# Optimization experiments

Measured on AMD Instinct MI355X. Metric: run time of the kernel, lower is better.

## Reference

```python
import jax, jax.numpy as jnp
import numpy as np

N_HEADS = 8


def setup_inputs() -> dict:
    key = jax.random.key(0)
    qkv = jax.random.normal(key, (4, 1536, 2048), dtype=jnp.float32)
    return {"qkv": qkv}


def reference(qkv):
    bs, width, length = qkv.shape
    assert width % (3 * N_HEADS) == 0
    ch = width // (3 * N_HEADS)
    q, k, v = jnp.split(qkv, 3, axis=1)            # each [bs, H*C, T]
    scale = 1.0 / (ch ** 0.25)                      # 1/sqrt(sqrt(ch)) applied to both q and k
    q = (q * scale).reshape(bs * N_HEADS, ch, length)
    k = (k * scale).reshape(bs * N_HEADS, ch, length)
    v = v.reshape(bs * N_HEADS, ch, length)
    weight = jnp.einsum('bct,bcs->bts', q, k)       # [bs*H, T, T]
    weight = jax.nn.softmax(weight.astype(jnp.float32), axis=-1).astype(weight.dtype)
    a = jnp.einsum('bts,bcs->bct', weight, v)       # [bs*H, C, T]
    return a.reshape(bs, -1, length)
```

## Files before the change

kernel.cpp:

```cpp
#include <hip/hip_runtime.h>


typedef _Float16 half8  __attribute__((ext_vector_type(8)));
typedef _Float16 half4  __attribute__((ext_vector_type(4)));
typedef float    floatx4 __attribute__((ext_vector_type(4)));

constexpr int T   = 2048;
constexpr int TQ  = 128;
constexpr int TS  = 64;
constexpr int LDK = 72;
constexpr int LDV = 72;
constexpr int LDP = 72;
constexpr int NIT = T / TS;
constexpr float QSCALE = 0.125f * 1.44269504088896340736f;

__device__ __forceinline__ float pick4(float t0, float t1, float t2, float t3, int rr) {
    return (rr & 2) ? ((rr & 1) ? t3 : t2) : ((rr & 1) ? t1 : t0);
}
__device__ __forceinline__ half4 pack4(float a, float b, float c, float d) {
    half4 r;
    r[0] = (_Float16)a; r[1] = (_Float16)b;
    r[2] = (_Float16)c; r[3] = (_Float16)d;
    return r;
}

__global__ __launch_bounds__(512, 4)
void qkv_attn_kernel(const float* __restrict__ qkv, float* __restrict__ out) {
    __shared__ __align__(16) _Float16 sK[2][TS * LDK];
    __shared__ __align__(16) _Float16 sV[2][64 * LDV];
    __shared__ __align__(16) _Float16 sP[TQ * LDP];

    const int tid  = threadIdx.x;
    const int wave = tid >> 6;
    const int lane = tid & 63;
    const int n16  = lane & 15;
    const int quad = lane >> 4;

    const int bx = blockIdx.x;
    const int h  = bx & 31;
    const int qt = bx >> 5;
    const int b  = h >> 3;
    const int hh = h & 7;
    const int q0 = qt * TQ;

    const float* __restrict__ qbase = qkv + (size_t)(b * 1536 + hh * 64) * T;
    const float* __restrict__ kbase = qkv + (size_t)(b * 1536 + 512 + hh * 64) * T;
    const float* __restrict__ vbase = qkv + (size_t)(b * 1536 + 1024 + hh * 64) * T;
    float* __restrict__ obase = out + (size_t)(b * 512 + hh * 64) * T;

    const bool producer = wave >= 4;

    const int ptid = tid & 255;
    const int ks   = ((ptid >> 6) << 4) | (ptid & 15);
    const int kc4  = ((ptid >> 4) & 3) << 2;
    const int vc   = ptid >> 4;
    const int vs4  = (ptid & 15) << 2;

    auto stage = [&](int buf, int s0) {
        _Float16* kd = &sK[buf][ks * LDK];
        const float* kg = kbase + s0 + ks;
#pragma unroll
        for (int i = 0; i < 4; ++i) {
            const int c = i * 16 + kc4;
            const float f0 = kg[(c + 0) * T];
            const float f1 = kg[(c + 1) * T];
            const float f2 = kg[(c + 2) * T];
            const float f3 = kg[(c + 3) * T];
            *(half4*)&kd[c] = pack4(f0, f1, f2, f3);
        }
        const float* vg = vbase + vc * T + s0 + vs4;
        _Float16* vd = &sV[buf][vc * LDV + vs4];
#pragma unroll
        for (int i = 0; i < 4; ++i) {
            const floatx4 vv = *(const floatx4*)&vg[i * 16 * T];
            *(half4*)&vd[i * 16 * LDV] = pack4(vv.x, vv.y, vv.z, vv.w);
        }
    };

    half8 aq[2][2];
    floatx4 oacc[4][2];
    float lsum[2][4];

    if (!producer) {
#pragma unroll
        for (int qtile = 0; qtile < 2; ++qtile) {
            const int q = q0 + wave * 32 + qtile * 16 + n16;
#pragma unroll
            for (int kc = 0; kc < 2; ++kc)
#pragma unroll
                for (int j = 0; j < 8; ++j) {
                    const int c = kc * 32 + quad * 8 + j;
                    aq[qtile][kc][j] = (_Float16)(qbase[c * T + q] * QSCALE);
                }
        }
#pragma unroll
        for (int mt = 0; mt < 4; ++mt)
#pragma unroll
            for (int qtile = 0; qtile < 2; ++qtile) oacc[mt][qtile] = (floatx4)(0.f);
#pragma unroll
        for (int qtile = 0; qtile < 2; ++qtile)
#pragma unroll
            for (int r = 0; r < 4; ++r) lsum[qtile][r] = 0.f;
    }

    if (producer) stage(0, 0);
    __syncthreads();

    for (int it = 0; it < NIT; ++it) {
        const int buf = it & 1;
        if (producer) {
            if (it + 1 < NIT) stage(buf ^ 1, (it + 1) * TS);
        } else {
            const _Float16* kb = &sK[buf][0];
            const _Float16* vb = &sV[buf][0];
#pragma unroll
            for (int qtile = 0; qtile < 2; ++qtile) {
                floatx4 sacc[4];
#pragma unroll
                for (int stile = 0; stile < 4; ++stile) {
                    const half8 bk0 = *(const half8*)&kb[(stile * 16 + n16) * LDK + quad * 8];
                    const half8 bk1 = *(const half8*)&kb[(stile * 16 + n16) * LDK + 32 + quad * 8];
                    floatx4 acc = (floatx4)(0.f);
                    acc = __builtin_amdgcn_mfma_f32_16x16x32_f16(aq[qtile][0], bk0, acc, 0, 0, 0);
                    acc = __builtin_amdgcn_mfma_f32_16x16x32_f16(aq[qtile][1], bk1, acc, 0, 0, 0);
                    sacc[stile] = acc;
                }
#pragma unroll
                for (int stile = 0; stile < 4; ++stile)
#pragma unroll
                    for (int r = 0; r < 4; ++r) {
                        const float pv = __builtin_amdgcn_exp2f(sacc[stile][r]);
                        lsum[qtile][r] += pv;
                        sP[(wave * 32 + qtile * 16 + quad * 4 + r) * LDP + stile * 16 + n16] =
                            (_Float16)pv;
                    }
            }
#pragma unroll
            for (int kc = 0; kc < 2; ++kc) {
                const half8 bp0 = *(const half8*)&sP[(wave * 32 + n16) * LDP + kc * 32 + quad * 8];
                const half8 bp1 = *(const half8*)&sP[(wave * 32 + 16 + n16) * LDP + kc * 32 + quad * 8];
#pragma unroll
                for (int mt = 0; mt < 4; ++mt) {
                    const half8 av = *(const half8*)&vb[(mt * 16 + n16) * LDV + kc * 32 + quad * 8];
                    oacc[mt][0] = __builtin_amdgcn_mfma_f32_16x16x32_f16(av, bp0, oacc[mt][0], 0, 0, 0);
                    oacc[mt][1] = __builtin_amdgcn_mfma_f32_16x16x32_f16(av, bp1, oacc[mt][1], 0, 0, 0);
                }
            }
        }
        __syncthreads();
    }

    if (!producer) {
#pragma unroll
        for (int qtile = 0; qtile < 2; ++qtile) {
            float l0 = lsum[qtile][0], l1 = lsum[qtile][1];
            float l2 = lsum[qtile][2], l3 = lsum[qtile][3];
#pragma unroll
            for (int msk = 1; msk < 16; msk <<= 1) {
                l0 += __shfl_xor(l0, msk);
                l1 += __shfl_xor(l1, msk);
                l2 += __shfl_xor(l2, msk);
                l3 += __shfl_xor(l3, msk);
            }
            const int srcl = (n16 >> 2) << 4;
            const float t0 = __shfl(l0, srcl);
            const float t1 = __shfl(l1, srcl);
            const float t2 = __shfl(l2, srcl);
            const float t3 = __shfl(l3, srcl);
            const float linv = 1.0f / pick4(t0, t1, t2, t3, n16 & 3);
            const int tcol = q0 + wave * 32 + qtile * 16 + n16;
#pragma unroll
            for (int mt = 0; mt < 4; ++mt)
#pragma unroll
                for (int r = 0; r < 4; ++r)
                    obase[(mt * 16 + quad * 4 + r) * T + tcol] = oacc[mt][qtile][r] * linv;
        }
    }
}

extern "C" void kernel_launch(void* const* d_in, const int* in_sizes, int n_in,
                              void* d_out, int out_size, void* d_ws, size_t ws_size,
                              hipStream_t stream) {
    const float* qkv = (const float*)d_in[0];
    float* out = (float*)d_out;
    qkv_attn_kernel<<<dim3(512), dim3(512), 0, stream>>>(qkv, out);
}
```

Before: 132.3 us.

## Keep softmax probabilities in registers by transposing the QK^T MFMA operand order

```diff
diff --git a/kernel.cpp b/kernel.cpp
--- a/kernel.cpp
+++ b/kernel.cpp
@@ -10,13 +10,9 @@
 constexpr int TS  = 64;
 constexpr int LDK = 72;
 constexpr int LDV = 72;
-constexpr int LDP = 72;
 constexpr int NIT = T / TS;
 constexpr float QSCALE = 0.125f * 1.44269504088896340736f;
 
-__device__ __forceinline__ float pick4(float t0, float t1, float t2, float t3, int rr) {
-    return (rr & 2) ? ((rr & 1) ? t3 : t2) : ((rr & 1) ? t1 : t0);
-}
 __device__ __forceinline__ half4 pack4(float a, float b, float c, float d) {
     half4 r;
     r[0] = (_Float16)a; r[1] = (_Float16)b;
@@ -28,13 +24,12 @@
 void qkv_attn_kernel(const float* __restrict__ qkv, float* __restrict__ out) {
     __shared__ __align__(16) _Float16 sK[2][TS * LDK];
     __shared__ __align__(16) _Float16 sV[2][64 * LDV];
-    __shared__ __align__(16) _Float16 sP[TQ * LDP];
 
     const int tid  = threadIdx.x;
     const int wave = tid >> 6;
     const int lane = tid & 63;
     const int n16  = lane & 15;
-    const int quad = lane >> 4;
+    const int g    = lane >> 4;
 
     const int bx = blockIdx.x;
     const int h  = bx & 31;
@@ -77,30 +72,27 @@
         }
     };
 
-    half8 aq[2][2];
+    half8 bq[2][2];
     floatx4 oacc[4][2];
-    float lsum[2][4];
+    float lsum[2];
 
     if (!producer) {
 #pragma unroll
-        for (int qtile = 0; qtile < 2; ++qtile) {
-            const int q = q0 + wave * 32 + qtile * 16 + n16;
+        for (int qt2 = 0; qt2 < 2; ++qt2) {
+            const int q = q0 + wave * 32 + qt2 * 16 + n16;
 #pragma unroll
-            for (int kc = 0; kc < 2; ++kc)
+            for (int kcA = 0; kcA < 2; ++kcA)
 #pragma unroll
                 for (int j = 0; j < 8; ++j) {
-                    const int c = kc * 32 + quad * 8 + j;
-                    aq[qtile][kc][j] = (_Float16)(qbase[c * T + q] * QSCALE);
+                    const int c = kcA * 32 + g * 8 + j;
+                    bq[qt2][kcA][j] = (_Float16)(qbase[c * T + q] * QSCALE);
                 }
         }
 #pragma unroll
         for (int mt = 0; mt < 4; ++mt)
 #pragma unroll
-            for (int qtile = 0; qtile < 2; ++qtile) oacc[mt][qtile] = (floatx4)(0.f);
-#pragma unroll
-        for (int qtile = 0; qtile < 2; ++qtile)
-#pragma unroll
-            for (int r = 0; r < 4; ++r) lsum[qtile][r] = 0.f;
+            for (int qt2 = 0; qt2 < 2; ++qt2) oacc[mt][qt2] = (floatx4)(0.f);
+        lsum[0] = 0.f; lsum[1] = 0.f;
     }
 
     if (producer) stage(0, 0);
@@ -114,36 +106,47 @@
             const _Float16* kb = &sK[buf][0];
             const _Float16* vb = &sV[buf][0];
 #pragma unroll
-            for (int qtile = 0; qtile < 2; ++qtile) {
-                floatx4 sacc[4];
+            for (int kc2 = 0; kc2 < 2; ++kc2) {
+                floatx4 sacc[2][2];
 #pragma unroll
-                for (int stile = 0; stile < 4; ++stile) {
-                    const half8 bk0 = *(const half8*)&kb[(stile * 16 + n16) * LDK + quad * 8];
-                    const half8 bk1 = *(const half8*)&kb[(stile * 16 + n16) * LDK + 32 + quad * 8];
-                    floatx4 acc = (floatx4)(0.f);
-                    acc = __builtin_amdgcn_mfma_f32_16x16x32_f16(aq[qtile][0], bk0, acc, 0, 0, 0);
-                    acc = __builtin_amdgcn_mfma_f32_16x16x32_f16(aq[qtile][1], bk1, acc, 0, 0, 0);
-                    sacc[stile] = acc;
+                for (int sub = 0; sub < 2; ++sub) {
+                    const int stile = kc2 * 2 + sub;
+                    const half8 ak0 = *(const half8*)&kb[(stile * 16 + n16) * LDK + g * 8];
+                    const half8 ak1 = *(const half8*)&kb[(stile * 16 + n16) * LDK + 32 + g * 8];
+#pragma unroll
+                    for (int qt2 = 0; qt2 < 2; ++qt2) {
+                        floatx4 acc = (floatx4)(0.f);
+                        acc = __builtin_amdgcn_mfma_f32_16x16x32_f16(ak0, bq[qt2][0], acc, 0, 0, 0);
+                        acc = __builtin_amdgcn_mfma_f32_16x16x32_f16(ak1, bq[qt2][1], acc, 0, 0, 0);
+                        sacc[qt2][sub] = acc;
+                    }
+                }
+                half8 av[4];
+#pragma unroll
+                for (int mt = 0; mt < 4; ++mt) {
+                    const _Float16* vr = &vb[(mt * 16 + n16) * LDV + kc2 * 32];
+                    const half4 lo = *(const half4*)&vr[g * 4];
+                    const half4 hi = *(const half4*)&vr[16 + g * 4];
+                    av[mt][0] = lo[0]; av[mt][1] = lo[1]; av[mt][2] = lo[2]; av[mt][3] = lo[3];
+                    av[mt][4] = hi[0]; av[mt][5] = hi[1]; av[mt][6] = hi[2]; av[mt][7] = hi[3];
                 }
 #pragma unroll
-                for (int stile = 0; stile < 4; ++stile)
+                for (int qt2 = 0; qt2 < 2; ++qt2) {
+                    float pv[8];
 #pragma unroll
-                    for (int r = 0; r < 4; ++r) {
-                        const float pv = __builtin_amdgcn_exp2f(sacc[stile][r]);
-                        lsum[qtile][r] += pv;
-                        sP[(wave * 32 + qtile * 16 + quad * 4 + r) * LDP + stile * 16 + n16] =
-                            (_Float16)pv;
-                    }
-            }
+                    for (int sub = 0; sub < 2; ++sub)
 #pragma unroll
-            for (int kc = 0; kc < 2; ++kc) {
-                const half8 bp0 = *(const half8*)&sP[(wave * 32 + n16) * LDP + kc * 32 + quad * 8];
-                const half8 bp1 = *(const half8*)&sP[(wave * 32 + 16 + n16) * LDP + kc * 32 + quad * 8];
+                        for (int r = 0; r < 4; ++r)
+                            pv[sub * 4 + r] = __builtin_amdgcn_exp2f(sacc[qt2][sub][r]);
+                    lsum[qt2] += ((pv[0] + pv[1]) + (pv[2] + pv[3]))
+                               + ((pv[4] + pv[5]) + (pv[6] + pv[7]));
+                    half8 bp;
 #pragma unroll
-                for (int mt = 0; mt < 4; ++mt) {
-                    const half8 av = *(const half8*)&vb[(mt * 16 + n16) * LDV + kc * 32 + quad * 8];
-                    oacc[mt][0] = __builtin_amdgcn_mfma_f32_16x16x32_f16(av, bp0, oacc[mt][0], 0, 0, 0);
-                    oacc[mt][1] = __builtin_amdgcn_mfma_f32_16x16x32_f16(av, bp1, oacc[mt][1], 0, 0, 0);
+                    for (int i = 0; i < 8; ++i) bp[i] = (_Float16)pv[i];
+#pragma unroll
+                    for (int mt = 0; mt < 4; ++mt)
+                        oacc[mt][qt2] = __builtin_amdgcn_mfma_f32_16x16x32_f16(
+                            av[mt], bp, oacc[mt][qt2], 0, 0, 0);
                 }
             }
         }
@@ -152,28 +155,17 @@
 
     if (!producer) {
 #pragma unroll
-        for (int qtile = 0; qtile < 2; ++qtile) {
-            float l0 = lsum[qtile][0], l1 = lsum[qtile][1];
-            float l2 = lsum[qtile][2], l3 = lsum[qtile][3];
-#pragma unroll
-            for (int msk = 1; msk < 16; msk <<= 1) {
-                l0 += __shfl_xor(l0, msk);
-                l1 += __shfl_xor(l1, msk);
-                l2 += __shfl_xor(l2, msk);
-                l3 += __shfl_xor(l3, msk);
-            }
-            const int srcl = (n16 >> 2) << 4;
-            const float t0 = __shfl(l0, srcl);
-            const float t1 = __shfl(l1, srcl);
-            const float t2 = __shfl(l2, srcl);
-            const float t3 = __shfl(l3, srcl);
-            const float linv = 1.0f / pick4(t0, t1, t2, t3, n16 & 3);
-            const int tcol = q0 + wave * 32 + qtile * 16 + n16;
+        for (int qt2 = 0; qt2 < 2; ++qt2) {
+            float l = lsum[qt2];
+            l += __shfl_xor(l, 16);
+            l += __shfl_xor(l, 32);
+            const float linv = 1.0f / l;
+            const int tcol = q0 + wave * 32 + qt2 * 16 + n16;
 #pragma unroll
             for (int mt = 0; mt < 4; ++mt)
 #pragma unroll
                 for (int r = 0; r < 4; ++r)
-                    obase[(mt * 16 + quad * 4 + r) * T + tcol] = oacc[mt][qtile][r] * linv;
+                    obase[(mt * 16 + g * 4 + r) * T + tcol] = oacc[mt][qt2][r] * linv;
         }
     }
 }
```

Result: faster. 124.7 us (-5.8%).
